# Performance work log

Measured on AMD Instinct MI355X. Metric: run time of the kernel, lower is better.

Reference implementation:

```python
import jax, jax.numpy as jnp
import numpy as np
from jax import lax

H = W = 128            # feature map spatial size (2h x 2w)
WIN = 16               # attention window size
DIM = 512
HEADS = 8
DIM_HEAD = 64
INNER = HEADS * DIM_HEAD
SCALE = DIM_HEAD ** -0.5
KEEP = 44
IOU_T = 0.2

_s = np.arange(0, H - WIN + 1, WIN // 2)
_sx, _sy = np.meshgrid(_s, _s)
WINDOWS = np.stack([_sx.ravel(), _sy.ravel(), _sx.ravel() + WIN - 1, _sy.ravel() + WIN - 1], 1).astype(np.float32)
M = WINDOWS.shape[0]   # 225
SX = jnp.asarray(WINDOWS[:, 0].astype(np.int32))
SY = jnp.asarray(WINDOWS[:, 1].astype(np.int32))

# ---- static pairwise IoU (torchvision convention: area=(x2-x1)*(y2-y1)) ----
_x1, _y1, _x2, _y2 = WINDOWS[:, 0], WINDOWS[:, 1], WINDOWS[:, 2], WINDOWS[:, 3]
_area = (_x2 - _x1) * (_y2 - _y1)
_iw = np.clip(np.minimum(_x2[:, None], _x2[None]) - np.maximum(_x1[:, None], _x1[None]), 0, None)
_ih = np.clip(np.minimum(_y2[:, None], _y2[None]) - np.maximum(_y1[:, None], _y1[None]), 0, None)
_inter = _iw * _ih
IOU = jnp.asarray((_inter / (_area[:, None] + _area[None] - _inter)).astype(np.float32))

# ---- roi_align (aligned=False, 1 sample/bin) == separable bilinear resample ----
_bin = (WIN - 1.0) / WIN
_r = (np.arange(WIN) + 0.5) * _bin
_q = np.floor(_r).astype(int)
_f = _r - _q
_A = np.zeros((WIN, WIN), np.float32)
_A[np.arange(WIN), _q] = 1.0 - _f
_A[np.arange(WIN), np.minimum(_q + 1, WIN - 1)] += _f
BILIN = jnp.asarray(_A)


def _nms_select(score):
    """Greedy NMS over the static window set; return first KEEP kept indices."""
    order = jnp.argsort(-score)
    iou_s = IOU[order][:, order]
    def body(i, supp):
        return supp | ((~supp[i]) & (iou_s[i] > IOU_T) & (jnp.arange(M) > i))
    supp = lax.fori_loop(0, M, body, jnp.zeros((M,), dtype=bool))
    pos = jnp.where(~supp, jnp.arange(M), M)
    pos = jnp.minimum(jnp.sort(pos)[:KEEP], M - 1)
    return order[pos]


def setup_inputs() -> dict:
    key = jax.random.key(0)
    k1, k2, k3, k4 = jax.random.split(key, 4)
    x = jax.random.normal(k1, (8, H * W, DIM), dtype=jnp.float32)
    prob = jax.random.uniform(k2, (8, 4, H // 2, W // 2), dtype=jnp.float32)
    W_fix = jnp.ones((1, 1, WIN // 2, WIN // 2), jnp.float32)   # FixCNN ones kernel
    W_qkv = jax.random.normal(k3, (3 * INNER, DIM), jnp.float32) * 0.02
    W_out = jax.random.normal(k4, (DIM, INNER), jnp.float32) * 0.02
    b_out = jnp.zeros((DIM,), jnp.float32)
    return {"x": x, "prob": prob, "W_fix": W_fix, "W_qkv": W_qkv, "W_out": W_out, "b_out": b_out}


def reference(x, prob, W_fix, W_qkv, W_out, b_out):
    b = x.shape[0]
    # entropy over class channels
    entropy = -jnp.sum(prob * jnp.log2(prob + 1e-10), axis=1)           # (b, 64, 64)
    # FixCNN: ones 8x8 kernel, stride 4, then /64
    score = lax.conv(entropy[:, None], W_fix, (WIN // 4, WIN // 4), 'VALID')
    score = (score / float((WIN // 2) ** 2)).reshape(b, -1)             # (b, M)
    x2d = x.transpose(0, 2, 1).reshape(b, DIM, H, W)                    # b d h w
    rng = jnp.arange(WIN)

    def per_batch(feat, sc):
        idx = _nms_select(sc)                                           # (KEEP,)
        sy, sx = SY[idx], SX[idx]
        # gather integer 16x16 patches (box corners are integers)
        patches = jax.vmap(lambda y, xc: lax.dynamic_slice(feat, (0, y, xc), (DIM, WIN, WIN)))(sy, sx)
        # roi_align bilinear resample (separable)
        pat = jnp.einsum('pi,mdij,qj->mdpq', BILIN, patches, BILIN)     # (KEEP, d, 16, 16)
        xi = pat.transpose(0, 2, 3, 1).reshape(KEEP, WIN * WIN, DIM)    # m n d
        qkv = xi @ W_qkv.T
        q, k, v = jnp.split(qkv, 3, axis=-1)
        to_h = lambda t: t.reshape(KEEP, WIN * WIN, HEADS, DIM_HEAD).transpose(0, 2, 1, 3)
        q, k, v = to_h(q), to_h(k), to_h(v)
        attn = jax.nn.softmax(jnp.einsum('mhnd,mhkd->mhnk', q, k) * SCALE, axis=-1)
        out = jnp.einsum('mhnk,mhkd->mhnd', attn, v)
        out = out.transpose(0, 2, 1, 3).reshape(KEEP, WIN * WIN, INNER)
        out = out @ W_out.T + b_out                                     # (KEEP, n, DIM)
        out2d = out.reshape(KEEP, WIN, WIN, DIM).transpose(0, 3, 1, 2)  # m d h w
        yy = sy[:, None, None] + rng[None, :, None]                     # (KEEP,16,1)
        xx = sx[:, None, None] + rng[None, None, :]                     # (KEEP,1,16)
        acc = jnp.zeros((DIM, H, W), x.dtype).at[:, yy, xx].add(out2d.transpose(1, 0, 2, 3))
        cnt = jnp.zeros((H, W), x.dtype).at[yy, xx].add(1.0)
        return acc, cnt

    acc, cnt = jax.vmap(per_batch)(x2d, score)
    outx = (acc / (cnt[:, None] + 1e-10)).reshape(b, DIM, H * W).transpose(0, 2, 1)
    return x + outx
```

## Files before the change

### kernel.cpp

```cpp
#include <hip/hip_runtime.h>
#include <type_traits>
#include <utility>

typedef unsigned short u16;
typedef __attribute__((ext_vector_type(8))) short short8;
typedef __attribute__((ext_vector_type(8))) __bf16 bf16v8;
typedef __attribute__((ext_vector_type(4))) float f32x4;
typedef __attribute__((ext_vector_type(16))) float f32x16;

template <typename T, typename = void> struct mfma_ok : std::false_type {};
template <typename T>
struct mfma_ok<T, std::void_t<decltype(__builtin_amdgcn_mfma_f32_16x16x32_bf16(
    std::declval<T>(), std::declval<T>(), std::declval<f32x4>(), 0, 0, 0))>>
    : std::true_type {};
using frag8 = std::conditional_t<mfma_ok<bf16v8>::value, bf16v8, short8>;

#define MFMA16(a, b, c) __builtin_amdgcn_mfma_f32_16x16x32_bf16((a), (b), (c), 0, 0, 0)
#define MFMA32(a, b, c) __builtin_amdgcn_mfma_f32_32x32x16_bf16((a), (b), (c), 0, 0, 0)

__device__ __forceinline__ float bf2f(u16 u) {
  unsigned v = ((unsigned)u) << 16;
  return __builtin_bit_cast(float, v);
}
__device__ __forceinline__ u16 f2bf(float f) {
  unsigned u = __builtin_bit_cast(unsigned, f);
  u = (u + 0x7fffu + ((u >> 16) & 1u)) >> 16;
  return (u16)u;
}
__device__ __forceinline__ unsigned cvtpk_bf16(float lo, float hi) {
  unsigned r;
  asm("v_cvt_pk_bf16_f32 %0, %1, %2" : "=v"(r) : "v"(lo), "v"(hi));
  return r;
}
__device__ __forceinline__ void gl16(const u16* g, u16* l) {
  __builtin_amdgcn_global_load_lds((__attribute__((address_space(1))) void*)(g),
                                   (__attribute__((address_space(3))) void*)(l), 16, 0, 0);
}
__device__ __forceinline__ void vmw8() { asm volatile("s_waitcnt vmcnt(8)" ::: "memory"); }
__device__ __forceinline__ void vmw0() { asm volatile("s_waitcnt vmcnt(0)" ::: "memory"); }
__device__ __forceinline__ void lgw0() { asm volatile("s_waitcnt lgkmcnt(0)" ::: "memory"); }

__global__ void k_score(const float* __restrict__ prob, const float* __restrict__ wfix,
                        float* __restrict__ scores) {
  const int b = blockIdx.x, tid = threadIdx.x;
  __shared__ float ent[64 * 64];
  __shared__ float wf[64];
  if (tid < 64) wf[tid] = wfix[tid];
  const float* pb = prob + (size_t)b * 4 * 4096;
  for (int p = tid; p < 4096; p += 256) {
    float e = 0.f;
#pragma unroll
    for (int ch = 0; ch < 4; ++ch) {
      float v = pb[ch * 4096 + p];
      e -= v * log2f(v + 1e-10f);
    }
    ent[p] = e;
  }
  __syncthreads();
  if (tid < 225) {
    int wy = tid / 15, wx = tid % 15;
    float s = 0.f;
    for (int a = 0; a < 8; ++a)
      for (int c = 0; c < 8; ++c)
        s += ent[(wy * 4 + a) * 64 + wx * 4 + c] * wf[a * 8 + c];
    scores[b * 225 + tid] = s * (1.0f / 64.0f);
  }
}

__device__ __forceinline__ float iou_pair(int wa, int wb) {
  float x1a = (float)((wa % 15) * 8), y1a = (float)((wa / 15) * 8);
  float x1b = (float)((wb % 15) * 8), y1b = (float)((wb / 15) * 8);
  float iw = fminf(x1a, x1b) + 15.f - fmaxf(x1a, x1b);
  float ih = fminf(y1a, y1b) + 15.f - fmaxf(y1a, y1b);
  iw = fmaxf(iw, 0.f);
  ih = fmaxf(ih, 0.f);
  float inter = iw * ih;
  return inter / (450.f - inter);
}

__global__ void k_nms(const float* __restrict__ scores, int* __restrict__ sel,
                      int* __restrict__ kept, float* __restrict__ mult) {
  const int b = blockIdx.x, t = threadIdx.x;
  __shared__ float s[225];
  __shared__ int order[225];
  __shared__ unsigned char supp[225];
  __shared__ int idx44[44];
  __shared__ int ks[225];
  __shared__ float ml[225];
  if (t < 225) s[t] = scores[b * 225 + t];
  __syncthreads();
  if (t < 225) {
    float st = s[t];
    int r = 0;
    for (int j = 0; j < 225; ++j) {
      float sj = s[j];
      r += (sj > st) || (sj == st && j < t);
    }
    order[r] = t;
    supp[t] = 0;
    ks[t] = -1;
    ml[t] = 0.f;
  }
  __syncthreads();
  for (int i = 0; i < 224; ++i) {
    if (t > i && t < 225 && !supp[i]) {
      if (iou_pair(order[i], order[t]) > 0.2f) supp[t] = 1;
    }
    __syncthreads();
  }
  if (t == 0) {
    int k = 0;
    for (int i = 0; i < 225 && k < 44; ++i)
      if (!supp[i]) idx44[k++] = order[i];
    while (k < 44) idx44[k++] = order[224];
    for (int k2 = 0; k2 < 44; ++k2) {
      int w = idx44[k2];
      if (ks[w] < 0) ks[w] = k2;
      ml[w] += 1.f;
    }
  }
  __syncthreads();
  if (t < 225) {
    kept[b * 225 + t] = ks[t];
    mult[b * 225 + t] = ml[t];
  }
  if (t < 44) sel[b * 44 + t] = idx44[t];
}

__global__ void k_castw(const float* __restrict__ Wq, const float* __restrict__ Wo,
                        u16* __restrict__ wqb, u16* __restrict__ wob) {
  int idx = blockIdx.x * 256 + threadIdx.x;
  if (idx < 786432) wqb[idx] = f2bf(Wq[idx]);
  int i2 = idx - 786432;
  if (i2 >= 0 && i2 < 262144) wob[i2] = f2bf(Wo[i2]);
}

__global__ __launch_bounds__(256) void k_gather(const float* __restrict__ x,
                                                const int* __restrict__ sel,
                                                u16* __restrict__ xi) {
  const size_t idx = (size_t)blockIdx.x * 256 + threadIdx.x;
  const int dc = (int)(idx & 63);
  const int pq = (int)((idx >> 6) & 255);
  const int g = (int)(idx >> 14);
  const int b = g / 44;
  const int w = sel[g];
  const int sy = (w / 15) * 8, sx = (w % 15) * 8;
  const int p = pq >> 4, q = pq & 15;
  float rp = ((float)p + 0.5f) * 0.9375f;
  int i0 = (int)rp;
  float fp = rp - (float)i0;
  float rq = ((float)q + 0.5f) * 0.9375f;
  int j0 = (int)rq;
  float fq = rq - (float)j0;
  const float w00 = (1.f - fp) * (1.f - fq), w01 = (1.f - fp) * fq;
  const float w10 = fp * (1.f - fq), w11 = fp * fq;
  const float* xb = x + ((size_t)b * 16384 + (size_t)(sy + i0) * 128 + sx + j0) * 512 + dc * 8;
  const float4* t00 = (const float4*)xb;
  const float4* t01 = (const float4*)(xb + 512);
  const float4* t10 = (const float4*)(xb + 512 * 128);
  const float4* t11 = (const float4*)(xb + 512 * 129);
  float acc[8];
#pragma unroll
  for (int h = 0; h < 2; ++h) {
    float4 a = t00[h], bb = t01[h], c = t10[h], d = t11[h];
    acc[h * 4 + 0] = w00 * a.x + w01 * bb.x + w10 * c.x + w11 * d.x;
    acc[h * 4 + 1] = w00 * a.y + w01 * bb.y + w10 * c.y + w11 * d.y;
    acc[h * 4 + 2] = w00 * a.z + w01 * bb.z + w10 * c.z + w11 * d.z;
    acc[h * 4 + 3] = w00 * a.w + w01 * bb.w + w10 * c.w + w11 * d.w;
  }
  short8 o;
#pragma unroll
  for (int e = 0; e < 8; ++e) o[e] = (short)f2bf(acc[e]);
  *(short8*)&xi[((size_t)g * 256 + pq) * 512 + dc * 8] = o;
}

template <int BIAS>
__global__ __launch_bounds__(512, 2) void k_gemm256(const u16* __restrict__ A,
                                                    const u16* __restrict__ B, u16* __restrict__ C,
                                                    const float* __restrict__ bias, int M, int N,
                                                    int K, int nbn) {
  __shared__ u16 sA[2][256 * 64];
  __shared__ u16 sB[2][256 * 64];
  const int tid = threadIdx.x, lane = tid & 63, wv = tid >> 6;
  const int f = blockIdx.x;
  const int q8 = gridDim.x >> 3;
  const int wg = (f & 7) * q8 + (f >> 3);
  const int bm = wg / nbn, bn = wg % nbn;
  const int wm = (wv >> 2) * 128, wn = (wv & 3) * 64;
  const int l15 = lane & 15, k8 = (lane >> 4) * 8;
  const int xorv = (l15 & 7) * 8;
  const int srow = tid >> 3;
  const int sc8 = ((tid ^ (tid >> 3)) & 7) * 8;
  const u16* Ab = A + (size_t)(bm * 256 + srow) * K + sc8;
  const u16* Bb = B + (size_t)(bn * 256 + srow) * K + sc8;

  f32x4 acc[8][4] = {};

#define STAGE(kt, buf)                                                       \
  {                                                                          \
    const int ko = (kt) * 64;                                                \
    _Pragma("unroll") for (int c = 0; c < 4; ++c) {                          \
      gl16(Ab + (size_t)(c * 64) * K + ko, &sA[buf][c * 4096 + wv * 512]);   \
      gl16(Bb + (size_t)(c * 64) * K + ko, &sB[buf][c * 4096 + wv * 512]);   \
    }                                                                        \
  }

  STAGE(0, 0);
  STAGE(1, 1);

  for (int t = 0; t < 8; ++t) {
    const int buf = t & 1;
    if (t == 7)
      vmw0();
    else
      vmw8();
    __builtin_amdgcn_sched_barrier(0);
    __builtin_amdgcn_s_barrier();
#pragma unroll
    for (int mh = 0; mh < 2; ++mh)
#pragma unroll
      for (int nh = 0; nh < 2; ++nh) {
        frag8 af[4][2], bf[2][2];
#pragma unroll
        for (int i = 0; i < 4; ++i)
#pragma unroll
          for (int kk = 0; kk < 2; ++kk)
            af[i][kk] = *(const frag8*)&sA[buf][(wm + (mh * 4 + i) * 16 + l15) * 64 +
                                               ((kk * 32 + k8) ^ xorv)];
#pragma unroll
        for (int j = 0; j < 2; ++j)
#pragma unroll
          for (int kk = 0; kk < 2; ++kk)
            bf[j][kk] = *(const frag8*)&sB[buf][(wn + (nh * 2 + j) * 16 + l15) * 64 +
                                               ((kk * 32 + k8) ^ xorv)];
        __builtin_amdgcn_s_setprio(1);
#pragma unroll
        for (int i = 0; i < 4; ++i)
#pragma unroll
          for (int j = 0; j < 2; ++j)
#pragma unroll
            for (int kk = 0; kk < 2; ++kk)
              acc[mh * 4 + i][nh * 2 + j] = MFMA16(af[i][kk], bf[j][kk], acc[mh * 4 + i][nh * 2 + j]);
        __builtin_amdgcn_s_setprio(0);
      }
    lgw0();
    __builtin_amdgcn_sched_barrier(0);
    __builtin_amdgcn_s_barrier();
    if (t < 6) STAGE(t + 2, buf);
  }
#undef STAGE

  const int cc = lane & 15, rr = (lane >> 4) * 4;
#pragma unroll
  for (int i = 0; i < 8; ++i)
#pragma unroll
    for (int j = 0; j < 4; ++j) {
      int col = bn * 256 + wn + j * 16 + cc;
      float badd = BIAS ? bias[col] : 0.f;
#pragma unroll
      for (int e = 0; e < 4; ++e) {
        int row = bm * 256 + wm + i * 16 + rr + e;
        C[(size_t)row * N + col] = f2bf(acc[i][j][e] + badd);
      }
    }
}

__global__ __launch_bounds__(256, 2) void k_attn(const u16* __restrict__ qkv,
                                                 u16* __restrict__ aout) {
  const int g = blockIdx.x;
  const int win = g >> 3, h = g & 7;
  const int tid = threadIdx.x, lane = tid & 63, wv = tid >> 6;
  const int l31 = lane & 31, l5 = lane >> 5;
  const bool lo32 = (lane < 32);
  __shared__ u16 smem[25344];
  u16* KbB = smem;
  u16* VtB = smem + 8704;
  const u16* base = qkv + (size_t)win * 256 * 1536;
  const u16* kbase = base + 512 + h * 64;
  const u16* vbase = base + 1024 + h * 64;
  const int prow = tid >> 2, pc16 = (tid & 3) * 16;

  {
    const u16* kp = kbase + (size_t)prow * 1536 + pc16;
    *(short8*)&KbB[prow * 68 + pc16] = *(const short8*)kp;
    *(short8*)&KbB[prow * 68 + pc16 + 8] = *(const short8*)(kp + 8);
  }
  {
    const u16* vp = vbase + (size_t)tid * 1536;
#pragma unroll
    for (int c8 = 0; c8 < 64; c8 += 8) {
      short8 v = *(const short8*)(vp + c8);
#pragma unroll
      for (int e2 = 0; e2 < 8; ++e2) VtB[(c8 + e2) * 260 + tid] = (u16)v[e2];
    }
  }
  frag8 qf[2][4];
#pragma unroll
  for (int qt = 0; qt < 2; ++qt)
#pragma unroll
    for (int c = 0; c < 4; ++c)
      qf[qt][c] = *(const frag8*)(base + (size_t)(wv * 64 + qt * 32 + l31) * 1536 + h * 64 +
                                  c * 16 + l5 * 8);
  __syncthreads();

  f32x16 of[2][2] = {};
  float m_run[2] = {-3e38f, -3e38f};
  float l_run[2] = {0.f, 0.f};

  int cur = 0;
  for (int kb = 0; kb < 4; ++kb) {
    short8 pf0 = {}, pf1 = {};
    if (kb < 3) {
      const u16* kp = kbase + (size_t)((kb + 1) * 64 + prow) * 1536 + pc16;
      pf0 = *(const short8*)kp;
      pf1 = *(const short8*)(kp + 8);
    }
#pragma unroll
    for (int qt = 0; qt < 2; ++qt) {
      f32x16 s0 = {}, s1 = {};
#pragma unroll
      for (int c = 0; c < 4; ++c) {
        frag8 kf0 = *(const frag8*)&KbB[cur * 4352 + l31 * 68 + c * 16 + l5 * 8];
        frag8 kf1 = *(const frag8*)&KbB[cur * 4352 + (32 + l31) * 68 + c * 16 + l5 * 8];
        s0 = MFMA32(kf0, qf[qt][c], s0);
        s1 = MFMA32(kf1, qf[qt][c], s1);
      }
      float tm[16];
#pragma unroll
      for (int r = 0; r < 16; ++r) tm[r] = fmaxf(s0[r], s1[r]);
#pragma unroll
      for (int r = 0; r < 8; ++r) tm[r] = fmaxf(tm[r], tm[r + 8]);
#pragma unroll
      for (int r = 0; r < 4; ++r) tm[r] = fmaxf(tm[r], tm[r + 4]);
      float pm = fmaxf(fmaxf(tm[0], tm[1]), fmaxf(tm[2], tm[3]));
      pm = fmaxf(pm, __shfl_xor(pm, 32));
      if (!__all(pm <= m_run[qt] + 64.f)) {
        float mn = fmaxf(m_run[qt], pm);
        float corr = __expf((m_run[qt] - mn) * 0.125f);
        l_run[qt] *= corr;
#pragma unroll
        for (int dt = 0; dt < 2; ++dt)
#pragma unroll
          for (int r = 0; r < 16; ++r) of[qt][dt][r] *= corr;
        m_run[qt] = mn;
      }
      const float mqt = m_run[qt];
      float ls = 0.f;
#pragma unroll
      for (int kt = 0; kt < 2; ++kt) {
        const f32x16 sv = kt ? s1 : s0;
        float p[16];
#pragma unroll
        for (int r = 0; r < 16; ++r) p[r] = __expf((sv[r] - mqt) * 0.125f);
        float e0 = (p[0] + p[1]) + (p[2] + p[3]);
        float e1 = (p[4] + p[5]) + (p[6] + p[7]);
        float e2 = (p[8] + p[9]) + (p[10] + p[11]);
        float e3 = (p[12] + p[13]) + (p[14] + p[15]);
        ls += (e0 + e1) + (e2 + e3);
#pragma unroll
        for (int cc = 0; cc < 2; ++cc) {
          const int bx = cc * 8;
          unsigned a0 = cvtpk_bf16(p[bx + 0], p[bx + 1]);
          unsigned a1 = cvtpk_bf16(p[bx + 2], p[bx + 3]);
          unsigned b0 = cvtpk_bf16(p[bx + 4], p[bx + 5]);
          unsigned b1 = cvtpk_bf16(p[bx + 6], p[bx + 7]);
          unsigned sa0 = __shfl_xor(a0, 32);
          unsigned sa1 = __shfl_xor(a1, 32);
          unsigned sb0 = __shfl_xor(b0, 32);
          unsigned sb1 = __shfl_xor(b1, 32);
          uint4 fu;
          fu.x = lo32 ? a0 : sb0;
          fu.y = lo32 ? a1 : sb1;
          fu.z = lo32 ? sa0 : b0;
          fu.w = lo32 ? sa1 : b1;
          frag8 pb = __builtin_bit_cast(frag8, fu);
#pragma unroll
          for (int dt = 0; dt < 2; ++dt) {
            frag8 va = *(const frag8*)&VtB[(dt * 32 + l31) * 260 + kb * 64 + kt * 32 + cc * 16 +
                                           l5 * 8];
            of[qt][dt] = MFMA32(va, pb, of[qt][dt]);
          }
        }
      }
      l_run[qt] += ls;
    }
    if (kb < 3) {
      *(short8*)&KbB[(cur ^ 1) * 4352 + prow * 68 + pc16] = pf0;
      *(short8*)&KbB[(cur ^ 1) * 4352 + prow * 68 + pc16 + 8] = pf1;
    }
    __syncthreads();
    cur ^= 1;
  }

  float inv[2];
#pragma unroll
  for (int qt = 0; qt < 2; ++qt) {
    float lt = l_run[qt] + __shfl_xor(l_run[qt], 32);
    inv[qt] = 1.0f / lt;
  }
  u16* sc = smem + wv * 4352;
#pragma unroll
  for (int qt = 0; qt < 2; ++qt)
#pragma unroll
    for (int dt = 0; dt < 2; ++dt)
#pragma unroll
      for (int j = 0; j < 4; ++j) {
        unsigned w0 = cvtpk_bf16(of[qt][dt][4 * j + 0] * inv[qt], of[qt][dt][4 * j + 1] * inv[qt]);
        unsigned w1 = cvtpk_bf16(of[qt][dt][4 * j + 2] * inv[qt], of[qt][dt][4 * j + 3] * inv[qt]);
        *(uint2*)&sc[(qt * 32 + l31) * 68 + dt * 32 + 8 * j + 4 * l5] = make_uint2(w0, w1);
      }
  __syncthreads();
#pragma unroll
  for (int rep = 0; rep < 8; ++rep) {
    int row = rep * 8 + (lane >> 3);
    uint2 lo = *(const uint2*)&sc[row * 68 + (lane & 7) * 8];
    uint2 hi = *(const uint2*)&sc[row * 68 + (lane & 7) * 8 + 4];
    *(int4*)&aout[(size_t)(win * 256 + wv * 64 + row) * 512 + h * 64 + (lane & 7) * 8] =
        make_int4((int)lo.x, (int)lo.y, (int)hi.x, (int)hi.y);
  }
}

__global__ void k_final(const float* __restrict__ x, const u16* __restrict__ proj,
                        const int* __restrict__ kept, const float* __restrict__ mult,
                        float* __restrict__ out) {
  const size_t idx = (size_t)blockIdx.x * 256 + threadIdx.x;
  const int dci = (int)(idx & 31);
  const int pix = (int)((idx >> 5) & 16383);
  const int b = (int)(idx >> 19);
  const int y = pix >> 7, xc = pix & 127;
  float acc[16];
#pragma unroll
  for (int e = 0; e < 16; ++e) acc[e] = 0.f;
  float c = 0.f;
  const int wyh = y >> 3, wxh = xc >> 3;
#pragma unroll
  for (int a = 0; a < 2; ++a) {
    int wy = wyh - 1 + a;
    if (wy < 0 || wy > 14) continue;
#pragma unroll
    for (int bb = 0; bb < 2; ++bb) {
      int wx = wxh - 1 + bb;
      if (wx < 0 || wx > 14) continue;
      int w = wy * 15 + wx;
      int slot = kept[b * 225 + w];
      if (slot < 0) continue;
      float ml = mult[b * 225 + w];
      c += ml;
      const u16* pr = proj +
                      ((size_t)((b * 44 + slot) * 256 + (y - wy * 8) * 16 + (xc - wx * 8))) * 512 +
                      (size_t)dci * 16;
      short8 v0 = *(const short8*)pr;
      short8 v1 = *(const short8*)(pr + 8);
#pragma unroll
      for (int e = 0; e < 8; ++e) acc[e] += ml * bf2f((u16)v0[e]);
#pragma unroll
      for (int e = 0; e < 8; ++e) acc[8 + e] += ml * bf2f((u16)v1[e]);
    }
  }
  const float inv = 1.f / (c + 1e-10f);
  const size_t off = ((size_t)(b * 16384 + pix)) * 512 + (size_t)dci * 16;
  const float4* xp = (const float4*)(x + off);
  float4* op = (float4*)(out + off);
#pragma unroll
  for (int q4 = 0; q4 < 4; ++q4) {
    float4 xv = xp[q4];
    float4 ov;
    ov.x = xv.x + acc[q4 * 4 + 0] * inv;
    ov.y = xv.y + acc[q4 * 4 + 1] * inv;
    ov.z = xv.z + acc[q4 * 4 + 2] * inv;
    ov.w = xv.w + acc[q4 * 4 + 3] * inv;
    op[q4] = ov;
  }
}

extern "C" void kernel_launch(void* const* d_in, const int* in_sizes, int n_in, void* d_out,
                              int out_size, void* d_ws, size_t ws_size, hipStream_t stream) {
  const float* x = (const float*)d_in[0];
  const float* prob = (const float*)d_in[1];
  const float* wfix = (const float*)d_in[2];
  const float* Wq = (const float*)d_in[3];
  const float* Wo = (const float*)d_in[4];
  const float* bo = (const float*)d_in[5];
  float* out = (float*)d_out;
  char* ws = (char*)d_ws;

  float* scores = (float*)(ws + 0);
  int* sel = (int*)(ws + 8192);
  int* kept = (int*)(ws + 16384);
  float* mult = (float*)(ws + 24576);
  u16* wqb = (u16*)(ws + 32768);
  u16* wob = (u16*)(ws + 32768 + 1572864);
  u16* xi = (u16*)(ws + 4194304);
  u16* qkv = (u16*)(ws + 4194304 + 92274688);
  u16* aout = xi;
  u16* proj = qkv;

  k_score<<<8, 256, 0, stream>>>(prob, wfix, scores);
  k_nms<<<8, 256, 0, stream>>>(scores, sel, kept, mult);
  k_castw<<<4096, 256, 0, stream>>>(Wq, Wo, wqb, wob);
  k_gather<<<22528, 256, 0, stream>>>(x, sel, xi);
  k_gemm256<0><<<2112, 512, 0, stream>>>(xi, wqb, qkv, nullptr, 90112, 1536, 512, 6);
  k_attn<<<2816, 256, 0, stream>>>(qkv, aout);
  k_gemm256<1><<<704, 512, 0, stream>>>(aout, wob, proj, bo, 90112, 512, 512, 2);
  k_final<<<16384, 256, 0, stream>>>(x, proj, kept, mult, out);
}
```

Measured before the change: 742.2 us.

## Stream V in double-buffered tiles, raise attn occupancy, use permlane32 swap

The attention kernel stops staging the whole transposed V for a window up front. V is now loaded per 64-key block into a double-buffered LDS tile alongside K, which cuts shared memory use enough to raise launch bounds to 3 blocks per CU. The cross-half-wave exchange of P fragments now uses v_permlane32_swap instead of four shuffles plus selects. The GEMM inner loop hoists all A/B fragment loads per mh with a single LDS wait before the MFMAs. Risks: more syncs per K/V block, register pressure from the 3-wave-per-SIMD bound, and the epilogue relies on only a compiler barrier where a __syncthreads used to be.

Measured after the change: 734.9 us. About the same (-1.0%).

```diff
diff --git a/kernel.cpp b/kernel.cpp
--- a/kernel.cpp
+++ b/kernel.cpp
@@ -217,34 +217,37 @@
     __builtin_amdgcn_sched_barrier(0);
     __builtin_amdgcn_s_barrier();
 #pragma unroll
-    for (int mh = 0; mh < 2; ++mh)
-#pragma unroll
-      for (int nh = 0; nh < 2; ++nh) {
-        frag8 af[4][2], bf[2][2];
+    for (int mh = 0; mh < 2; ++mh) {
+      frag8 af[4][2], bf[2][2][2];
+#pragma unroll
+      for (int i = 0; i < 4; ++i)
+#pragma unroll
+        for (int kk = 0; kk < 2; ++kk)
+          af[i][kk] = *(const frag8*)&sA[buf][(wm + (mh * 4 + i) * 16 + l15) * 64 +
+                                             ((kk * 32 + k8) ^ xorv)];
+#pragma unroll
+      for (int nh = 0; nh < 2; ++nh)
+#pragma unroll
+        for (int j = 0; j < 2; ++j)
+#pragma unroll
+          for (int kk = 0; kk < 2; ++kk)
+            bf[nh][j][kk] = *(const frag8*)&sB[buf][(wn + (nh * 2 + j) * 16 + l15) * 64 +
+                                                    ((kk * 32 + k8) ^ xorv)];
+      lgw0();
+      __builtin_amdgcn_sched_barrier(0);
+      __builtin_amdgcn_s_setprio(1);
+#pragma unroll
+      for (int nh = 0; nh < 2; ++nh)
 #pragma unroll
         for (int i = 0; i < 4; ++i)
 #pragma unroll
-          for (int kk = 0; kk < 2; ++kk)
-            af[i][kk] = *(const frag8*)&sA[buf][(wm + (mh * 4 + i) * 16 + l15) * 64 +
-                                               ((kk * 32 + k8) ^ xorv)];
-#pragma unroll
-        for (int j = 0; j < 2; ++j)
-#pragma unroll
-          for (int kk = 0; kk < 2; ++kk)
-            bf[j][kk] = *(const frag8*)&sB[buf][(wn + (nh * 2 + j) * 16 + l15) * 64 +
-                                               ((kk * 32 + k8) ^ xorv)];
-        __builtin_amdgcn_s_setprio(1);
-#pragma unroll
-        for (int i = 0; i < 4; ++i)
-#pragma unroll
           for (int j = 0; j < 2; ++j)
 #pragma unroll
             for (int kk = 0; kk < 2; ++kk)
-              acc[mh * 4 + i][nh * 2 + j] = MFMA16(af[i][kk], bf[j][kk], acc[mh * 4 + i][nh * 2 + j]);
-        __builtin_amdgcn_s_setprio(0);
-      }
-    lgw0();
-    __builtin_amdgcn_sched_barrier(0);
+              acc[mh * 4 + i][nh * 2 + j] =
+                  MFMA16(af[i][kk], bf[nh][j][kk], acc[mh * 4 + i][nh * 2 + j]);
+      __builtin_amdgcn_s_setprio(0);
+    }
     __builtin_amdgcn_s_barrier();
     if (t < 6) STAGE(t + 2, buf);
   }
@@ -265,14 +268,13 @@
     }
 }
 
-__global__ __launch_bounds__(256, 2) void k_attn(const u16* __restrict__ qkv,
+__global__ __launch_bounds__(256, 3) void k_attn(const u16* __restrict__ qkv,
                                                  u16* __restrict__ aout) {
   const int g = blockIdx.x;
   const int win = g >> 3, h = g & 7;
   const int tid = threadIdx.x, lane = tid & 63, wv = tid >> 6;
   const int l31 = lane & 31, l5 = lane >> 5;
-  const bool lo32 = (lane < 32);
-  __shared__ u16 smem[25344];
+  __shared__ u16 smem[17664];
   u16* KbB = smem;
   u16* VtB = smem + 8704;
   const u16* base = qkv + (size_t)win * 256 * 1536;
@@ -280,20 +282,6 @@
   const u16* vbase = base + 1024 + h * 64;
   const int prow = tid >> 2, pc16 = (tid & 3) * 16;
 
-  {
-    const u16* kp = kbase + (size_t)prow * 1536 + pc16;
-    *(short8*)&KbB[prow * 68 + pc16] = *(const short8*)kp;
-    *(short8*)&KbB[prow * 68 + pc16 + 8] = *(const short8*)(kp + 8);
-  }
-  {
-    const u16* vp = vbase + (size_t)tid * 1536;
-#pragma unroll
-    for (int c8 = 0; c8 < 64; c8 += 8) {
-      short8 v = *(const short8*)(vp + c8);
-#pragma unroll
-      for (int e2 = 0; e2 < 8; ++e2) VtB[(c8 + e2) * 260 + tid] = (u16)v[e2];
-    }
-  }
   frag8 qf[2][4];
 #pragma unroll
   for (int qt = 0; qt < 2; ++qt)
@@ -301,6 +289,21 @@
     for (int c = 0; c < 4; ++c)
       qf[qt][c] = *(const frag8*)(base + (size_t)(wv * 64 + qt * 32 + l31) * 1536 + h * 64 +
                                   c * 16 + l5 * 8);
+  {
+    const u16* kp = kbase + (size_t)prow * 1536 + pc16;
+    short8 ka = *(const short8*)kp;
+    short8 kb2 = *(const short8*)(kp + 8);
+    const u16* vp = vbase + (size_t)prow * 1536 + pc16;
+    short8 va = *(const short8*)vp;
+    short8 vb2 = *(const short8*)(vp + 8);
+    *(short8*)&KbB[prow * 68 + pc16] = ka;
+    *(short8*)&KbB[prow * 68 + pc16 + 8] = kb2;
+#pragma unroll
+    for (int e = 0; e < 8; ++e) {
+      VtB[(pc16 + e) * 70 + prow] = (u16)va[e];
+      VtB[(pc16 + 8 + e) * 70 + prow] = (u16)vb2[e];
+    }
+  }
   __syncthreads();
 
   f32x16 of[2][2] = {};
@@ -309,11 +312,14 @@
 
   int cur = 0;
   for (int kb = 0; kb < 4; ++kb) {
-    short8 pf0 = {}, pf1 = {};
+    short8 pk0 = {}, pk1 = {}, pv0 = {}, pv1 = {};
     if (kb < 3) {
       const u16* kp = kbase + (size_t)((kb + 1) * 64 + prow) * 1536 + pc16;
-      pf0 = *(const short8*)kp;
-      pf1 = *(const short8*)(kp + 8);
+      pk0 = *(const short8*)kp;
+      pk1 = *(const short8*)(kp + 8);
+      const u16* vp = vbase + (size_t)((kb + 1) * 64 + prow) * 1536 + pc16;
+      pv0 = *(const short8*)vp;
+      pv1 = *(const short8*)(vp + 8);
     }
 #pragma unroll
     for (int qt = 0; qt < 2; ++qt) {
@@ -364,19 +370,17 @@
           unsigned a1 = cvtpk_bf16(p[bx + 2], p[bx + 3]);
           unsigned b0 = cvtpk_bf16(p[bx + 4], p[bx + 5]);
           unsigned b1 = cvtpk_bf16(p[bx + 6], p[bx + 7]);
-          unsigned sa0 = __shfl_xor(a0, 32);
-          unsigned sa1 = __shfl_xor(a1, 32);
-          unsigned sb0 = __shfl_xor(b0, 32);
-          unsigned sb1 = __shfl_xor(b1, 32);
+          asm("v_permlane32_swap_b32 %0, %1" : "+v"(a0), "+v"(b0));
+          asm("v_permlane32_swap_b32 %0, %1" : "+v"(a1), "+v"(b1));
           uint4 fu;
-          fu.x = lo32 ? a0 : sb0;
-          fu.y = lo32 ? a1 : sb1;
-          fu.z = lo32 ? sa0 : b0;
-          fu.w = lo32 ? sa1 : b1;
+          fu.x = a0;
+          fu.y = a1;
+          fu.z = b0;
+          fu.w = b1;
           frag8 pb = __builtin_bit_cast(frag8, fu);
 #pragma unroll
           for (int dt = 0; dt < 2; ++dt) {
-            frag8 va = *(const frag8*)&VtB[(dt * 32 + l31) * 260 + kb * 64 + kt * 32 + cc * 16 +
+            frag8 va = *(const frag8*)&VtB[cur * 4480 + (dt * 32 + l31) * 70 + kt * 32 + cc * 16 +
                                            l5 * 8];
             of[qt][dt] = MFMA32(va, pb, of[qt][dt]);
           }
@@ -385,8 +389,14 @@
       l_run[qt] += ls;
     }
     if (kb < 3) {
-      *(short8*)&KbB[(cur ^ 1) * 4352 + prow * 68 + pc16] = pf0;
-      *(short8*)&KbB[(cur ^ 1) * 4352 + prow * 68 + pc16 + 8] = pf1;
+      *(short8*)&KbB[(cur ^ 1) * 4352 + prow * 68 + pc16] = pk0;
+      *(short8*)&KbB[(cur ^ 1) * 4352 + prow * 68 + pc16 + 8] = pk1;
+      u16* vd = &VtB[(cur ^ 1) * 4480 + prow];
+#pragma unroll
+      for (int e = 0; e < 8; ++e) {
+        vd[(pc16 + e) * 70] = (u16)pv0[e];
+        vd[(pc16 + 8 + e) * 70] = (u16)pv1[e];
+      }
     }
     __syncthreads();
     cur ^= 1;
@@ -399,6 +409,7 @@
     inv[qt] = 1.0f / lt;
   }
   u16* sc = smem + wv * 4352;
+  __syncthreads();
 #pragma unroll
   for (int qt = 0; qt < 2; ++qt)
 #pragma unroll
@@ -409,7 +420,7 @@
         unsigned w1 = cvtpk_bf16(of[qt][dt][4 * j + 2] * inv[qt], of[qt][dt][4 * j + 3] * inv[qt]);
         *(uint2*)&sc[(qt * 32 + l31) * 68 + dt * 32 + 8 * j + 4 * l5] = make_uint2(w0, w1);
       }
-  __syncthreads();
+  asm volatile("" ::: "memory");
 #pragma unroll
   for (int rep = 0; rep < 8; ++rep) {
     int row = rep * 8 + (lane >> 3);
```
